# Optimization experiments

Hardware: AMD Instinct MI355X
Metric: run time of the kernel (lower is better)

Reference implementation:

```python
import jax, jax.numpy as jnp
import numpy as np
from functools import partial

N_NODES = 50000
N_EDGES = 1_600_000
T = 9
F_IN = 128
HID = 128
OUT = 1


def setup_inputs() -> dict:
    key = jax.random.key(0)
    ks = jax.random.split(key, 8)
    s = 0.05
    return {
        "x_seq": jax.random.normal(ks[0], (T, N_NODES, F_IN), dtype=jnp.float32),
        "edge_index": jax.random.randint(ks[1], (2, N_EDGES), 0, N_NODES, dtype=jnp.int64),
        "W_gcn": jax.random.normal(ks[2], (F_IN, HID), dtype=jnp.float32) * s,
        "b_gcn": jnp.zeros((HID,), dtype=jnp.float32),
        "W_ih": jax.random.normal(ks[3], (4 * HID, HID), dtype=jnp.float32) * s,
        "W_hh": jax.random.normal(ks[4], (4 * HID, HID), dtype=jnp.float32) * s,
        "b_ih": jnp.zeros((4 * HID,), dtype=jnp.float32),
        "b_hh": jnp.zeros((4 * HID,), dtype=jnp.float32),
        "W_fc": jax.random.normal(ks[5], (HID, OUT), dtype=jnp.float32) * s,
        "b_fc": jnp.zeros((OUT,), dtype=jnp.float32),
    }


def reference(x_seq, edge_index, W_gcn, b_gcn, W_ih, W_hh, b_ih, b_hh, W_fc, b_fc):
    T_, N, _ = x_seq.shape
    H = W_hh.shape[1]

    # --- GCNConv normalization (add self-loops, symmetric deg^-1/2) ---
    loops = jnp.arange(N, dtype=edge_index.dtype)
    src = jnp.concatenate([edge_index[0], loops])  # [E+N]
    dst = jnp.concatenate([edge_index[1], loops])  # [E+N]
    deg = jax.ops.segment_sum(jnp.ones_like(dst, dtype=x_seq.dtype), dst, num_segments=N)
    dinv = jnp.where(deg > 0, jax.lax.rsqrt(deg), 0.0)
    norm = dinv[src] * dinv[dst]  # [E+N]

    # Linear transform for all timesteps at once (dense GEMM)
    xw = jnp.einsum("tnf,fh->tnh", x_seq, W_gcn)  # [T, N, H]

    # Per-timestep gather -> scale -> scatter-add (scan to bound memory)
    def gcn_step(_, xw_t):
        msg = xw_t[src] * norm[:, None]                       # [E+N, H]
        agg = jax.ops.segment_sum(msg, dst, num_segments=N)   # [N, H]
        return None, jax.nn.relu(agg + b_gcn)                 # dropout: eval mode (identity)

    _, emb = jax.lax.scan(gcn_step, None, xw)  # [T, N, H]

    # --- single-layer LSTM over time, nodes as batch (PyTorch gate order i,f,g,o) ---
    def lstm_step(carry, x_t):
        h_prev, c_prev = carry
        gates = x_t @ W_ih.T + h_prev @ W_hh.T + (b_ih + b_hh)  # [N, 4H]
        i, f, g, o = jnp.split(gates, 4, axis=-1)
        i, f, o = jax.nn.sigmoid(i), jax.nn.sigmoid(f), jax.nn.sigmoid(o)
        g = jnp.tanh(g)
        c = f * c_prev + i * g
        h = o * jnp.tanh(c)
        return (h, c), h

    init = (jnp.zeros((N, H), x_seq.dtype), jnp.zeros((N, H), x_seq.dtype))
    _, hs = jax.lax.scan(lstm_step, init, emb)  # [T, N, H]

    lstm_out = jnp.transpose(hs, (1, 0, 2))  # [N, T, H] (batch_first)
    # final_dropout: eval mode (identity)
    return lstm_out @ W_fc + b_fc  # [N, T, OUT]
```

## Files before the change

### kernel.cpp

```cpp
#include <hip/hip_runtime.h>
#include <math.h>

#define NN 50000
#define TT 9
#define FD 128
#define HD 128

using short8 = __attribute__((ext_vector_type(8))) short;
using f32x4  = __attribute__((ext_vector_type(4))) float;
using half2v = __attribute__((ext_vector_type(2))) _Float16;
typedef unsigned short ushort_t;

__device__ inline unsigned short f2bf(float x) {
  unsigned int u = __float_as_uint(x);
  unsigned int r = (u + 0x7fffu + ((u >> 16) & 1u)) >> 16;
  return (unsigned short)r;
}
__device__ inline float bf2f(unsigned short h) {
  return __uint_as_float(((unsigned int)h) << 16);
}
__device__ inline void split2(float x, unsigned short& h, unsigned short& l) {
  h = f2bf(x);
  l = f2bf(x - bf2f(h));
}
__device__ inline float fast_sigmoid(float x) {
  x = fminf(fmaxf(x, -30.f), 30.f);
  return 1.f / (1.f + __expf(-x));
}
__device__ inline float fast_tanh(float x) {
  x = fminf(fmaxf(x, -15.f), 15.f);
  float e = __expf(2.f * x);
  return (e - 1.f) / (e + 1.f);
}

__global__ void k_detect(const unsigned int* __restrict__ e32, int nchk,
                         int* __restrict__ stride_out) {
  __shared__ unsigned int red[256];
  unsigned int acc = 0;
  for (int i = threadIdx.x; i < nchk; i += 256) acc |= e32[2 * i + 1];
  red[threadIdx.x] = acc;
  __syncthreads();
  for (int s = 128; s > 0; s >>= 1) {
    if ((int)threadIdx.x < s) red[threadIdx.x] |= red[threadIdx.x + s];
    __syncthreads();
  }
  if (threadIdx.x == 0) stride_out[0] = (red[0] == 0u) ? 2 : 1;
}

__global__ void k_count(const unsigned int* __restrict__ e32, int E,
                        const int* __restrict__ stridep, int* __restrict__ cnt) {
  int e = blockIdx.x * 256 + threadIdx.x;
  if (e >= E) return;
  int st = stridep[0];
  int d = (int)e32[(size_t)(E + e) * st];
  atomicAdd(&cnt[d], 1);
}

__global__ void k_dinv(const int* __restrict__ cnt, float* __restrict__ dinv, int N) {
  int n = blockIdx.x * 256 + threadIdx.x;
  if (n < N) dinv[n] = rsqrtf((float)(cnt[n] + 1));
}

__global__ void k_scan(const int* __restrict__ cnt, int* __restrict__ rowp, int N) {
  __shared__ int buf[1024];
  __shared__ int carry_s;
  if (threadIdx.x == 0) carry_s = 0;
  __syncthreads();
  for (int base = 0; base < N; base += 1024) {
    int i = base + threadIdx.x;
    int v = (i < N) ? cnt[i] : 0;
    buf[threadIdx.x] = v;
    __syncthreads();
    for (int off = 1; off < 1024; off <<= 1) {
      int t = ((int)threadIdx.x >= off) ? buf[threadIdx.x - off] : 0;
      __syncthreads();
      buf[threadIdx.x] += t;
      __syncthreads();
    }
    int incl = buf[threadIdx.x];
    int carry = carry_s;
    if (i < N) rowp[i] = carry + incl - v;
    __syncthreads();
    if (threadIdx.x == 1023) carry_s = carry + incl;
    __syncthreads();
  }
  if (threadIdx.x == 0) rowp[N] = carry_s;
}

__global__ void k_scatter(const unsigned int* __restrict__ e32, int E,
                          const int* __restrict__ stridep, const int* __restrict__ rowp,
                          int* __restrict__ fill, int* __restrict__ col) {
  int e = blockIdx.x * 256 + threadIdx.x;
  if (e >= E) return;
  int st = stridep[0];
  int s = (int)e32[(size_t)e * st];
  int d = (int)e32[(size_t)(E + e) * st];
  int pos = rowp[d] + atomicAdd(&fill[d], 1);
  col[pos] = s;
}

__global__ __launch_bounds__(256) void k_prep(const float* __restrict__ x,
                                              const float* __restrict__ dinv,
                                              _Float16* __restrict__ xs) {
  int lane = threadIdx.x & 63;
  int n = blockIdx.x * 4 + (threadIdx.x >> 6);
  int t = blockIdx.y;
  float dn = dinv[n];
  float2 v = *(const float2*)(x + ((size_t)t * NN + n) * 128 + lane * 2);
  half2v r;
  r.x = (_Float16)(v.x * dn);
  r.y = (_Float16)(v.y * dn);
  *(half2v*)(xs + ((size_t)t * NN + n) * 128 + lane * 2) = r;
}

__global__ void k_packw(const float* __restrict__ Wih, const float* __restrict__ Whh,
                        const float* __restrict__ bih, const float* __restrict__ bhh,
                        ushort_t* __restrict__ Wh_, ushort_t* __restrict__ Wl_,
                        float* __restrict__ bsum) {
  int r = blockIdx.x;
  int k = threadIdx.x;
  int ri = (r & 127) * 4 + (r >> 7);
  float v = (k < 128) ? Wih[(size_t)r * 128 + k] : Whh[(size_t)r * 128 + (k - 128)];
  unsigned short h, l;
  split2(v, h, l);
  size_t o = ((size_t)(k >> 3) * 512 + ri) * 8 + (k & 7);
  Wh_[o] = h;
  Wl_[o] = l;
  if (k == 0) bsum[ri] = bih[r] + bhh[r];
}

__global__ void k_packg(const float* __restrict__ Wg, ushort_t* __restrict__ Bh_,
                        ushort_t* __restrict__ Bl_) {
  int h = blockIdx.x, k = threadIdx.x;
  unsigned short hh, ll;
  split2(Wg[(size_t)k * 128 + h], hh, ll);
  size_t o = ((size_t)(k >> 3) * 128 + h) * 8 + (k & 7);
  Bh_[o] = hh;
  Bl_[o] = ll;
}

__global__ __launch_bounds__(256) void k_agg(const _Float16* __restrict__ xs,
                                             const float* __restrict__ dinv,
                                             const int* __restrict__ rowp,
                                             const int* __restrict__ col,
                                             ushort_t* __restrict__ agg_h,
                                             ushort_t* __restrict__ agg_l) {
  __shared__ unsigned int pk[4][128];
  int lane = threadIdx.x & 63;
  int wv = threadIdx.x >> 6;
  int n = blockIdx.x * 4 + wv;
  int t = blockIdx.y;
  const _Float16* xb = xs + (size_t)t * NN * 128;
  float dn = dinv[n];
  half2v sv = *(const half2v*)(xb + (size_t)n * 128 + lane * 2);
  float ax = (float)sv.x, ay = (float)sv.y;
  int beg = rowp[n], end = rowp[n + 1];
  for (int base = beg; base < end; base += 64) {
    int m = end - base;
    if (m > 64) m = 64;
    int sl = (lane < m) ? col[base + lane] : 0;
    int j = 0;
    for (; j + 8 <= m; j += 8) {
      int s[8];
#pragma unroll
      for (int u = 0; u < 8; ++u) s[u] = __shfl(sl, j + u);
      half2v g[8];
#pragma unroll
      for (int u = 0; u < 8; ++u)
        g[u] = *(const half2v*)(xb + (size_t)s[u] * 128 + lane * 2);
#pragma unroll
      for (int u = 0; u < 8; ++u) {
        ax += (float)g[u].x;
        ay += (float)g[u].y;
      }
    }
    for (; j < m; ++j) {
      int s = __shfl(sl, j);
      half2v g = *(const half2v*)(xb + (size_t)s * 128 + lane * 2);
      ax += (float)g.x;
      ay += (float)g.y;
    }
  }
  unsigned short hx, lx, hy, ly;
  split2(ax * dn, hx, lx);
  split2(ay * dn, hy, ly);
  pk[wv][lane * 2] = ((unsigned int)hx << 16) | lx;
  pk[wv][lane * 2 + 1] = ((unsigned int)hy << 16) | ly;
  __syncthreads();
  int tid = threadIdx.x;
  int chunk = tid >> 4, g = (tid >> 2) & 3, e2 = (tid & 3) * 2;
  unsigned int p0 = pk[g][chunk * 8 + e2];
  unsigned int p1 = pk[g][chunk * 8 + e2 + 1];
  int n2 = blockIdx.x * 4 + g;
  size_t ob = ((size_t)(chunk * 9 + t) * NN + n2) * 8 + e2;
  ushort2 vh, vl;
  vh.x = (unsigned short)(p0 >> 16);
  vh.y = (unsigned short)(p1 >> 16);
  vl.x = (unsigned short)(p0 & 0xffffu);
  vl.y = (unsigned short)(p1 & 0xffffu);
  *(ushort2*)(agg_h + ob) = vh;
  *(ushort2*)(agg_l + ob) = vl;
}

#define BN 48
__global__ __launch_bounds__(512, 4) void k_fused(
    const ushort_t* __restrict__ Ah_, const ushort_t* __restrict__ Al_,
    const ushort_t* __restrict__ Gh_, const ushort_t* __restrict__ Gl_,
    const float* __restrict__ bg, const ushort_t* __restrict__ Wh_,
    const ushort_t* __restrict__ Wl_, const float* __restrict__ bsum,
    const float* __restrict__ Wfc, const float* __restrict__ bfc,
    float* __restrict__ out) {
  __shared__ unsigned int ldsE[BN * 132];
  __shared__ unsigned int ldsH[BN * 132];
  __shared__ float obuf[8][BN];
  int tid = threadIdx.x;
  int w = tid >> 6, lane = tid & 63, q = lane >> 4, cl = lane & 15;
  int n0 = blockIdx.x * BN;
  const short8 zz = {0, 0, 0, 0, 0, 0, 0, 0};
  float cst[4][3] = {};
  float bfv = bfc[0];
#pragma unroll 1
  for (int t = 0; t < TT; ++t) {
    {
      f32x4 acce[3] = {};
#pragma unroll 1
      for (int ks = 0; ks < 4; ++ks) {
        int chunk = ks * 4 + q;
        size_t ao = ((size_t)chunk * 128 + w * 16 + cl) * 8;
        short8 gah = *(const short8*)(Gh_ + ao);
        short8 gal = *(const short8*)(Gl_ + ao);
#pragma unroll
        for (int ct = 0; ct < 3; ++ct) {
          int node = n0 + ct * 16 + cl;
          short8 bh = zz, bl = zz;
          if (node < NN) {
            size_t o = ((size_t)(chunk * 9 + t) * NN + node) * 8;
            bh = *(const short8*)(Ah_ + o);
            bl = *(const short8*)(Al_ + o);
          }
          acce[ct] = __builtin_amdgcn_mfma_f32_16x16x32_bf16(gah, bh, acce[ct], 0, 0, 0);
          acce[ct] = __builtin_amdgcn_mfma_f32_16x16x32_bf16(gah, bl, acce[ct], 0, 0, 0);
          acce[ct] = __builtin_amdgcn_mfma_f32_16x16x32_bf16(gal, bh, acce[ct], 0, 0, 0);
        }
      }
#pragma unroll
      for (int ct = 0; ct < 3; ++ct) {
#pragma unroll
        for (int j = 0; j < 4; ++j) {
          int hid = w * 16 + q * 4 + j;
          float v = acce[ct][j] + bg[hid];
          v = v > 0.f ? v : 0.f;
          unsigned short hh, hl;
          split2(v, hh, hl);
          ldsE[(ct * 16 + cl) * 132 + hid] = ((unsigned int)hh << 16) | hl;
        }
      }
    }
    __syncthreads();
    f32x4 acc[4][3] = {};
    int ksmax = (t == 0) ? 4 : 8;
#pragma unroll 1
    for (int ks = 0; ks < ksmax; ++ks) {
      int chunk = ks * 4 + q;
      const unsigned int* ldsB = (ks < 4) ? ldsE : ldsH;
      int kk = (ks & 3) * 32 + q * 8;
      short8 bh[3], bl[3];
#pragma unroll
      for (int ct = 0; ct < 3; ++ct) {
        const uint4* hp = (const uint4*)&ldsB[(ct * 16 + cl) * 132 + kk];
        uint4 ua = hp[0], ub = hp[1];
        union { unsigned int u[4]; short8 s; } rh, rl;
        rh.u[0] = __builtin_amdgcn_perm(ua.y, ua.x, 0x07060302u);
        rh.u[1] = __builtin_amdgcn_perm(ua.w, ua.z, 0x07060302u);
        rh.u[2] = __builtin_amdgcn_perm(ub.y, ub.x, 0x07060302u);
        rh.u[3] = __builtin_amdgcn_perm(ub.w, ub.z, 0x07060302u);
        rl.u[0] = __builtin_amdgcn_perm(ua.y, ua.x, 0x05040100u);
        rl.u[1] = __builtin_amdgcn_perm(ua.w, ua.z, 0x05040100u);
        rl.u[2] = __builtin_amdgcn_perm(ub.y, ub.x, 0x05040100u);
        rl.u[3] = __builtin_amdgcn_perm(ub.w, ub.z, 0x05040100u);
        bh[ct] = rh.s;
        bl[ct] = rl.s;
      }
#pragma unroll
      for (int rt = 0; rt < 4; ++rt) {
        size_t ao = ((size_t)chunk * 512 + w * 64 + rt * 16 + cl) * 8;
        short8 ah = *(const short8*)(Wh_ + ao);
        short8 al = *(const short8*)(Wl_ + ao);
#pragma unroll
        for (int ct = 0; ct < 3; ++ct) {
          acc[rt][ct] = __builtin_amdgcn_mfma_f32_16x16x32_bf16(ah, bh[ct], acc[rt][ct], 0, 0, 0);
          acc[rt][ct] = __builtin_amdgcn_mfma_f32_16x16x32_bf16(ah, bl[ct], acc[rt][ct], 0, 0, 0);
          acc[rt][ct] = __builtin_amdgcn_mfma_f32_16x16x32_bf16(al, bh[ct], acc[rt][ct], 0, 0, 0);
        }
      }
    }
    __syncthreads();
    float op[3] = {0.f, 0.f, 0.f};
#pragma unroll
    for (int rt = 0; rt < 4; ++rt) {
      int jl = w * 16 + rt * 4 + q;
      float4 bs = *(const float4*)(bsum + jl * 4);
      float wf = Wfc[jl];
#pragma unroll
      for (int ct = 0; ct < 3; ++ct) {
        float gi = acc[rt][ct][0] + bs.x;
        float gf = acc[rt][ct][1] + bs.y;
        float gg = acc[rt][ct][2] + bs.z;
        float go = acc[rt][ct][3] + bs.w;
        float ig = fast_sigmoid(gi), fg = fast_sigmoid(gf), og = fast_sigmoid(go);
        float gt = fast_tanh(gg);
        float cn = fg * cst[rt][ct] + ig * gt;
        cst[rt][ct] = cn;
        float hn = og * fast_tanh(cn);
        op[ct] += hn * wf;
        unsigned short hh, hl;
        split2(hn, hh, hl);
        ldsH[(ct * 16 + cl) * 132 + jl] = ((unsigned int)hh << 16) | hl;
      }
    }
#pragma unroll
    for (int ct = 0; ct < 3; ++ct) {
      op[ct] += __shfl_xor(op[ct], 16);
      op[ct] += __shfl_xor(op[ct], 32);
    }
    if (q == 0) {
#pragma unroll
      for (int ct = 0; ct < 3; ++ct) obuf[w][ct * 16 + cl] = op[ct];
    }
    __syncthreads();
    if (tid < BN) {
      int node = n0 + tid;
      if (node < NN) {
        float v = bfv;
#pragma unroll
        for (int ww = 0; ww < 8; ++ww) v += obuf[ww][tid];
        out[(size_t)node * TT + t] = v;
      }
    }
  }
}

static inline size_t alignup(size_t x) { return (x + 511) & ~(size_t)511; }

extern "C" void kernel_launch(void* const* d_in, const int* in_sizes, int n_in,
                              void* d_out, int out_size, void* d_ws, size_t ws_size,
                              hipStream_t stream) {
  const float* x_seq = (const float*)d_in[0];
  const unsigned int* e32 = (const unsigned int*)d_in[1];
  const float* W_gcn = (const float*)d_in[2];
  const float* b_gcn = (const float*)d_in[3];
  const float* W_ih = (const float*)d_in[4];
  const float* W_hh = (const float*)d_in[5];
  const float* b_ih = (const float*)d_in[6];
  const float* b_hh = (const float*)d_in[7];
  const float* W_fc = (const float*)d_in[8];
  const float* b_fc = (const float*)d_in[9];
  float* out = (float*)d_out;

  const int N = NN;
  const int E = in_sizes[1] / 2;

  char* p = (char*)d_ws;
  int* stridep = (int*)p;                    p += 512;
  int* cnt = (int*)p;                        p += alignup((size_t)N * 4);
  int* rowp = (int*)p;                       p += alignup((size_t)(N + 1) * 4);
  int* col = (int*)p;                        p += alignup((size_t)E * 4);
  float* dinv = (float*)p;                   p += alignup((size_t)N * 4);
  _Float16* xs16 = (_Float16*)p;             p += alignup((size_t)9 * N * 128 * 2);
  ushort_t* agg_h = (ushort_t*)p;            p += alignup((size_t)16 * 9 * N * 8 * 2);
  ushort_t* agg_l = (ushort_t*)p;            p += alignup((size_t)16 * 9 * N * 8 * 2);
  ushort_t* wpkh = (ushort_t*)p;             p += alignup((size_t)32 * 512 * 8 * 2);
  ushort_t* wpkl = (ushort_t*)p;             p += alignup((size_t)32 * 512 * 8 * 2);
  ushort_t* wgth = (ushort_t*)p;             p += alignup((size_t)16 * 128 * 8 * 2);
  ushort_t* wgtl = (ushort_t*)p;             p += alignup((size_t)16 * 128 * 8 * 2);
  float* bsum = (float*)p;                   p += alignup((size_t)512 * 4);

  hipMemsetAsync(cnt, 0, (size_t)N * 4, stream);

  int nchk = E < 8192 ? E : 8192;
  k_detect<<<1, 256, 0, stream>>>(e32, nchk, stridep);
  k_count<<<(E + 255) / 256, 256, 0, stream>>>(e32, E, stridep, cnt);
  k_dinv<<<(N + 255) / 256, 256, 0, stream>>>(cnt, dinv, N);
  k_scan<<<1, 1024, 0, stream>>>(cnt, rowp, N);
  hipMemsetAsync(cnt, 0, (size_t)N * 4, stream);
  k_scatter<<<(E + 255) / 256, 256, 0, stream>>>(e32, E, stridep, rowp, cnt, col);
  k_prep<<<dim3(N / 4, 9), 256, 0, stream>>>(x_seq, dinv, xs16);
  k_packw<<<512, 256, 0, stream>>>(W_ih, W_hh, b_ih, b_hh, wpkh, wpkl, bsum);
  k_packg<<<128, 128, 0, stream>>>(W_gcn, wgth, wgtl);

  k_agg<<<dim3(N / 4, 9), 256, 0, stream>>>(xs16, dinv, rowp, col, agg_h, agg_l);
  k_fused<<<(N + BN - 1) / BN, 512, 0, stream>>>(agg_h, agg_l, wgth, wgtl, b_gcn,
                                                 wpkh, wpkl, bsum, W_fc, b_fc, out);
}
```

Measured before the change: 1.442 ms.

## Aggregate all timesteps per node in one pass and split LDS hi/lo buffers

```diff
diff --git a/kernel.cpp b/kernel.cpp
--- a/kernel.cpp
+++ b/kernel.cpp
@@ -8,6 +8,7 @@
 
 using short8 = __attribute__((ext_vector_type(8))) short;
 using f32x4  = __attribute__((ext_vector_type(4))) float;
+using f32x2  = __attribute__((ext_vector_type(2))) float;
 using half2v = __attribute__((ext_vector_type(2))) _Float16;
 typedef unsigned short ushort_t;
 
@@ -106,7 +107,8 @@
   int n = blockIdx.x * 4 + (threadIdx.x >> 6);
   int t = blockIdx.y;
   float dn = dinv[n];
-  float2 v = *(const float2*)(x + ((size_t)t * NN + n) * 128 + lane * 2);
+  f32x2 v = __builtin_nontemporal_load(
+      (const f32x2*)(x + ((size_t)t * NN + n) * 128 + lane * 2));
   half2v r;
   r.x = (_Float16)(v.x * dn);
   r.y = (_Float16)(v.y * dn);
@@ -145,64 +147,85 @@
                                              const int* __restrict__ col,
                                              ushort_t* __restrict__ agg_h,
                                              ushort_t* __restrict__ agg_l) {
-  __shared__ unsigned int pk[4][128];
+  __shared__ unsigned int pk[4][9][130];
   int lane = threadIdx.x & 63;
   int wv = threadIdx.x >> 6;
   int n = blockIdx.x * 4 + wv;
-  int t = blockIdx.y;
-  const _Float16* xb = xs + (size_t)t * NN * 128;
   float dn = dinv[n];
-  half2v sv = *(const half2v*)(xb + (size_t)n * 128 + lane * 2);
-  float ax = (float)sv.x, ay = (float)sv.y;
+  float ax[9], ay[9];
+  {
+    const _Float16* xrow = xs + (size_t)n * 128 + lane * 2;
+#pragma unroll
+    for (int t = 0; t < 9; ++t) {
+      half2v sv = *(const half2v*)(xrow + (size_t)t * NN * 128);
+      ax[t] = (float)sv.x;
+      ay[t] = (float)sv.y;
+    }
+  }
   int beg = rowp[n], end = rowp[n + 1];
   for (int base = beg; base < end; base += 64) {
     int m = end - base;
     if (m > 64) m = 64;
     int sl = (lane < m) ? col[base + lane] : 0;
     int j = 0;
-    for (; j + 8 <= m; j += 8) {
-      int s[8];
-#pragma unroll
-      for (int u = 0; u < 8; ++u) s[u] = __shfl(sl, j + u);
-      half2v g[8];
-#pragma unroll
-      for (int u = 0; u < 8; ++u)
-        g[u] = *(const half2v*)(xb + (size_t)s[u] * 128 + lane * 2);
-#pragma unroll
-      for (int u = 0; u < 8; ++u) {
-        ax += (float)g[u].x;
-        ay += (float)g[u].y;
-      }
-    }
-    for (; j < m; ++j) {
-      int s = __shfl(sl, j);
-      half2v g = *(const half2v*)(xb + (size_t)s * 128 + lane * 2);
-      ax += (float)g.x;
-      ay += (float)g.y;
-    }
-  }
-  unsigned short hx, lx, hy, ly;
-  split2(ax * dn, hx, lx);
-  split2(ay * dn, hy, ly);
-  pk[wv][lane * 2] = ((unsigned int)hx << 16) | lx;
-  pk[wv][lane * 2 + 1] = ((unsigned int)hy << 16) | ly;
+    for (; j + 2 <= m; j += 2) {
+      int s0 = __shfl(sl, j), s1 = __shfl(sl, j + 1);
+      const _Float16* r0 = xs + (size_t)s0 * 128 + lane * 2;
+      const _Float16* r1 = xs + (size_t)s1 * 128 + lane * 2;
+      half2v g0[9], g1[9];
+#pragma unroll
+      for (int t = 0; t < 9; ++t) g0[t] = *(const half2v*)(r0 + (size_t)t * NN * 128);
+#pragma unroll
+      for (int t = 0; t < 9; ++t) g1[t] = *(const half2v*)(r1 + (size_t)t * NN * 128);
+#pragma unroll
+      for (int t = 0; t < 9; ++t) {
+        ax[t] += (float)g0[t].x + (float)g1[t].x;
+        ay[t] += (float)g0[t].y + (float)g1[t].y;
+      }
+    }
+    if (j < m) {
+      int s0 = __shfl(sl, j);
+      const _Float16* r0 = xs + (size_t)s0 * 128 + lane * 2;
+      half2v g0[9];
+#pragma unroll
+      for (int t = 0; t < 9; ++t) g0[t] = *(const half2v*)(r0 + (size_t)t * NN * 128);
+#pragma unroll
+      for (int t = 0; t < 9; ++t) {
+        ax[t] += (float)g0[t].x;
+        ay[t] += (float)g0[t].y;
+      }
+    }
+  }
+#pragma unroll
+  for (int t = 0; t < 9; ++t) {
+    unsigned short hx, lx, hy, ly;
+    split2(ax[t] * dn, hx, lx);
+    split2(ay[t] * dn, hy, ly);
+    pk[wv][t][lane * 2] = ((unsigned int)hx << 16) | lx;
+    pk[wv][t][lane * 2 + 1] = ((unsigned int)hy << 16) | ly;
+  }
   __syncthreads();
-  int tid = threadIdx.x;
-  int chunk = tid >> 4, g = (tid >> 2) & 3, e2 = (tid & 3) * 2;
-  unsigned int p0 = pk[g][chunk * 8 + e2];
-  unsigned int p1 = pk[g][chunk * 8 + e2 + 1];
-  int n2 = blockIdx.x * 4 + g;
-  size_t ob = ((size_t)(chunk * 9 + t) * NN + n2) * 8 + e2;
-  ushort2 vh, vl;
-  vh.x = (unsigned short)(p0 >> 16);
-  vh.y = (unsigned short)(p1 >> 16);
-  vl.x = (unsigned short)(p0 & 0xffffu);
-  vl.y = (unsigned short)(p1 & 0xffffu);
-  *(ushort2*)(agg_h + ob) = vh;
-  *(ushort2*)(agg_l + ob) = vl;
+  int n0 = blockIdx.x * 4;
+  for (int u = threadIdx.x; u < 576; u += 256) {
+    int g = u & 3, chunk = (u >> 2) & 15, t = u >> 6;
+    const unsigned int* src = &pk[g][t][chunk * 8];
+    unsigned int p[8];
+#pragma unroll
+    for (int e = 0; e < 8; ++e) p[e] = src[e];
+    union { unsigned int u4[4]; short8 s; } rh, rl;
+#pragma unroll
+    for (int k2 = 0; k2 < 4; ++k2) {
+      rh.u4[k2] = __builtin_amdgcn_perm(p[2 * k2 + 1], p[2 * k2], 0x07060302u);
+      rl.u4[k2] = __builtin_amdgcn_perm(p[2 * k2 + 1], p[2 * k2], 0x05040100u);
+    }
+    size_t o = ((size_t)(chunk * 9 + t) * NN + n0 + g) * 8;
+    __builtin_nontemporal_store(rh.s, (short8*)(agg_h + o));
+    __builtin_nontemporal_store(rl.s, (short8*)(agg_l + o));
+  }
 }
 
 #define BN 48
+#define LST 136
 __global__ __launch_bounds__(512, 4) void k_fused(
     const ushort_t* __restrict__ Ah_, const ushort_t* __restrict__ Al_,
     const ushort_t* __restrict__ Gh_, const ushort_t* __restrict__ Gl_,
@@ -210,8 +233,10 @@
     const ushort_t* __restrict__ Wl_, const float* __restrict__ bsum,
     const float* __restrict__ Wfc, const float* __restrict__ bfc,
     float* __restrict__ out) {
-  __shared__ unsigned int ldsE[BN * 132];
-  __shared__ unsigned int ldsH[BN * 132];
+  __shared__ ushort_t ldsEh[BN * LST];
+  __shared__ ushort_t ldsEl[BN * LST];
+  __shared__ ushort_t ldsHh[BN * LST];
+  __shared__ ushort_t ldsHl[BN * LST];
   __shared__ float obuf[8][BN];
   int tid = threadIdx.x;
   int w = tid >> 6, lane = tid & 63, q = lane >> 4, cl = lane & 15;
@@ -235,8 +260,8 @@
           short8 bh = zz, bl = zz;
           if (node < NN) {
             size_t o = ((size_t)(chunk * 9 + t) * NN + node) * 8;
-            bh = *(const short8*)(Ah_ + o);
-            bl = *(const short8*)(Al_ + o);
+            bh = __builtin_nontemporal_load((const short8*)(Ah_ + o));
+            bl = __builtin_nontemporal_load((const short8*)(Al_ + o));
           }
           acce[ct] = __builtin_amdgcn_mfma_f32_16x16x32_bf16(gah, bh, acce[ct], 0, 0, 0);
           acce[ct] = __builtin_amdgcn_mfma_f32_16x16x32_bf16(gah, bl, acce[ct], 0, 0, 0);
@@ -252,7 +277,9 @@
           v = v > 0.f ? v : 0.f;
           unsigned short hh, hl;
           split2(v, hh, hl);
-          ldsE[(ct * 16 + cl) * 132 + hid] = ((unsigned int)hh << 16) | hl;
+          int ro = (ct * 16 + cl) * LST + hid;
+          ldsEh[ro] = hh;
+          ldsEl[ro] = hl;
         }
       }
     }
@@ -262,24 +289,15 @@
 #pragma unroll 1
     for (int ks = 0; ks < ksmax; ++ks) {
       int chunk = ks * 4 + q;
-      const unsigned int* ldsB = (ks < 4) ? ldsE : ldsH;
+      const ushort_t* Bh = (ks < 4) ? ldsEh : ldsHh;
+      const ushort_t* Bl = (ks < 4) ? ldsEl : ldsHl;
       int kk = (ks & 3) * 32 + q * 8;
       short8 bh[3], bl[3];
 #pragma unroll
       for (int ct = 0; ct < 3; ++ct) {
-        const uint4* hp = (const uint4*)&ldsB[(ct * 16 + cl) * 132 + kk];
-        uint4 ua = hp[0], ub = hp[1];
-        union { unsigned int u[4]; short8 s; } rh, rl;
-        rh.u[0] = __builtin_amdgcn_perm(ua.y, ua.x, 0x07060302u);
-        rh.u[1] = __builtin_amdgcn_perm(ua.w, ua.z, 0x07060302u);
-        rh.u[2] = __builtin_amdgcn_perm(ub.y, ub.x, 0x07060302u);
-        rh.u[3] = __builtin_amdgcn_perm(ub.w, ub.z, 0x07060302u);
-        rl.u[0] = __builtin_amdgcn_perm(ua.y, ua.x, 0x05040100u);
-        rl.u[1] = __builtin_amdgcn_perm(ua.w, ua.z, 0x05040100u);
-        rl.u[2] = __builtin_amdgcn_perm(ub.y, ub.x, 0x05040100u);
-        rl.u[3] = __builtin_amdgcn_perm(ub.w, ub.z, 0x05040100u);
-        bh[ct] = rh.s;
-        bl[ct] = rl.s;
+        int ro = (ct * 16 + cl) * LST + kk;
+        bh[ct] = *(const short8*)(Bh + ro);
+        bl[ct] = *(const short8*)(Bl + ro);
       }
 #pragma unroll
       for (int rt = 0; rt < 4; ++rt) {
@@ -315,7 +333,9 @@
         op[ct] += hn * wf;
         unsigned short hh, hl;
         split2(hn, hh, hl);
-        ldsH[(ct * 16 + cl) * 132 + jl] = ((unsigned int)hh << 16) | hl;
+        int ro = (ct * 16 + cl) * LST + jl;
+        ldsHh[ro] = hh;
+        ldsHl[ro] = hl;
       }
     }
 #pragma unroll
@@ -388,7 +408,7 @@
   k_packw<<<512, 256, 0, stream>>>(W_ih, W_hh, b_ih, b_hh, wpkh, wpkl, bsum);
   k_packg<<<128, 128, 0, stream>>>(W_gcn, wgth, wgtl);
 
-  k_agg<<<dim3(N / 4, 9), 256, 0, stream>>>(xs16, dinv, rowp, col, agg_h, agg_l);
+  k_agg<<<N / 4, 256, 0, stream>>>(xs16, dinv, rowp, col, agg_h, agg_l);
   k_fused<<<(N + BN - 1) / BN, 512, 0, stream>>>(agg_h, agg_l, wgth, wgtl, b_gcn,
                                                  wpkh, wpkl, bsum, W_fc, b_fc, out);
 }
```

After: 1.619 ms. +12.2%, slower.

## Store aggregated features as single fp16 and widen fused LSTM tile to 96 nodes

Applied to the files above, without the earlier changes.

```diff
diff --git a/kernel.cpp b/kernel.cpp
--- a/kernel.cpp
+++ b/kernel.cpp
@@ -7,7 +7,9 @@
 #define HD 128
 
 using short8 = __attribute__((ext_vector_type(8))) short;
+using half8  = __attribute__((ext_vector_type(8))) _Float16;
 using f32x4  = __attribute__((ext_vector_type(4))) float;
+using f32x2  = __attribute__((ext_vector_type(2))) float;
 using half2v = __attribute__((ext_vector_type(2))) _Float16;
 typedef unsigned short ushort_t;
 
@@ -106,7 +108,8 @@
   int n = blockIdx.x * 4 + (threadIdx.x >> 6);
   int t = blockIdx.y;
   float dn = dinv[n];
-  float2 v = *(const float2*)(x + ((size_t)t * NN + n) * 128 + lane * 2);
+  f32x2 v = __builtin_nontemporal_load(
+      (const f32x2*)(x + ((size_t)t * NN + n) * 128 + lane * 2));
   half2v r;
   r.x = (_Float16)(v.x * dn);
   r.y = (_Float16)(v.y * dn);
@@ -129,23 +132,23 @@
   if (k == 0) bsum[ri] = bih[r] + bhh[r];
 }
 
-__global__ void k_packg(const float* __restrict__ Wg, ushort_t* __restrict__ Bh_,
-                        ushort_t* __restrict__ Bl_) {
+__global__ void k_packg(const float* __restrict__ Wg, _Float16* __restrict__ Gh_,
+                        _Float16* __restrict__ Gl_) {
   int h = blockIdx.x, k = threadIdx.x;
-  unsigned short hh, ll;
-  split2(Wg[(size_t)k * 128 + h], hh, ll);
+  float v = Wg[(size_t)k * 128 + h];
+  _Float16 hi = (_Float16)v;
+  _Float16 lo = (_Float16)(v - (float)hi);
   size_t o = ((size_t)(k >> 3) * 128 + h) * 8 + (k & 7);
-  Bh_[o] = hh;
-  Bl_[o] = ll;
+  Gh_[o] = hi;
+  Gl_[o] = lo;
 }
 
 __global__ __launch_bounds__(256) void k_agg(const _Float16* __restrict__ xs,
                                              const float* __restrict__ dinv,
                                              const int* __restrict__ rowp,
                                              const int* __restrict__ col,
-                                             ushort_t* __restrict__ agg_h,
-                                             ushort_t* __restrict__ agg_l) {
-  __shared__ unsigned int pk[4][128];
+                                             _Float16* __restrict__ agg16) {
+  __shared__ unsigned int pk[4][132];
   int lane = threadIdx.x & 63;
   int wv = threadIdx.x >> 6;
   int n = blockIdx.x * 4 + wv;
@@ -181,70 +184,66 @@
       ay += (float)g.y;
     }
   }
-  unsigned short hx, lx, hy, ly;
-  split2(ax * dn, hx, lx);
-  split2(ay * dn, hy, ly);
-  pk[wv][lane * 2] = ((unsigned int)hx << 16) | lx;
-  pk[wv][lane * 2 + 1] = ((unsigned int)hy << 16) | ly;
+  half2v r;
+  r.x = (_Float16)(ax * dn);
+  r.y = (_Float16)(ay * dn);
+  union { half2v h; unsigned int u; } cv;
+  cv.h = r;
+  pk[wv][lane] = cv.u;
   __syncthreads();
   int tid = threadIdx.x;
-  int chunk = tid >> 4, g = (tid >> 2) & 3, e2 = (tid & 3) * 2;
-  unsigned int p0 = pk[g][chunk * 8 + e2];
-  unsigned int p1 = pk[g][chunk * 8 + e2 + 1];
-  int n2 = blockIdx.x * 4 + g;
-  size_t ob = ((size_t)(chunk * 9 + t) * NN + n2) * 8 + e2;
-  ushort2 vh, vl;
-  vh.x = (unsigned short)(p0 >> 16);
-  vh.y = (unsigned short)(p1 >> 16);
-  vl.x = (unsigned short)(p0 & 0xffffu);
-  vl.y = (unsigned short)(p1 & 0xffffu);
-  *(ushort2*)(agg_h + ob) = vh;
-  *(ushort2*)(agg_l + ob) = vl;
-}
-
-#define BN 48
-__global__ __launch_bounds__(512, 4) void k_fused(
-    const ushort_t* __restrict__ Ah_, const ushort_t* __restrict__ Al_,
-    const ushort_t* __restrict__ Gh_, const ushort_t* __restrict__ Gl_,
-    const float* __restrict__ bg, const ushort_t* __restrict__ Wh_,
-    const ushort_t* __restrict__ Wl_, const float* __restrict__ bsum,
-    const float* __restrict__ Wfc, const float* __restrict__ bfc,
-    float* __restrict__ out) {
-  __shared__ unsigned int ldsE[BN * 132];
-  __shared__ unsigned int ldsH[BN * 132];
+  if (tid < 64) {
+    int g = tid & 3, c = tid >> 2;
+    uint4 u4;
+    u4.x = pk[g][c * 4 + 0];
+    u4.y = pk[g][c * 4 + 1];
+    u4.z = pk[g][c * 4 + 2];
+    u4.w = pk[g][c * 4 + 3];
+    int n2 = blockIdx.x * 4 + g;
+    *(uint4*)(agg16 + ((size_t)(c * 9 + t) * NN + n2) * 8) = u4;
+  }
+}
+
+#define BN 96
+#define LST 136
+__global__ __launch_bounds__(512, 2) void k_fused(
+    const _Float16* __restrict__ agg16, const _Float16* __restrict__ Gh_,
+    const _Float16* __restrict__ Gl_, const float* __restrict__ bg,
+    const ushort_t* __restrict__ Wh_, const ushort_t* __restrict__ Wl_,
+    const float* __restrict__ bsum, const float* __restrict__ Wfc,
+    const float* __restrict__ bfc, float* __restrict__ out) {
+  __shared__ ushort_t ldsEh[BN * LST];
+  __shared__ ushort_t ldsEl[BN * LST];
+  __shared__ ushort_t ldsHh[BN * LST];
+  __shared__ ushort_t ldsHl[BN * LST];
   __shared__ float obuf[8][BN];
   int tid = threadIdx.x;
   int w = tid >> 6, lane = tid & 63, q = lane >> 4, cl = lane & 15;
   int n0 = blockIdx.x * BN;
-  const short8 zz = {0, 0, 0, 0, 0, 0, 0, 0};
-  float cst[4][3] = {};
+  float cst[4][6] = {};
   float bfv = bfc[0];
 #pragma unroll 1
   for (int t = 0; t < TT; ++t) {
     {
-      f32x4 acce[3] = {};
-#pragma unroll 1
+      f32x4 acce[6] = {};
+#pragma unroll 2
       for (int ks = 0; ks < 4; ++ks) {
         int chunk = ks * 4 + q;
-        size_t ao = ((size_t)chunk * 128 + w * 16 + cl) * 8;
-        short8 gah = *(const short8*)(Gh_ + ao);
-        short8 gal = *(const short8*)(Gl_ + ao);
-#pragma unroll
-        for (int ct = 0; ct < 3; ++ct) {
+        size_t wo = ((size_t)chunk * 128 + w * 16 + cl) * 8;
+        half8 gah = *(const half8*)(Gh_ + wo);
+        half8 gal = *(const half8*)(Gl_ + wo);
+#pragma unroll
+        for (int ct = 0; ct < 6; ++ct) {
           int node = n0 + ct * 16 + cl;
-          short8 bh = zz, bl = zz;
-          if (node < NN) {
-            size_t o = ((size_t)(chunk * 9 + t) * NN + node) * 8;
-            bh = *(const short8*)(Ah_ + o);
-            bl = *(const short8*)(Al_ + o);
-          }
-          acce[ct] = __builtin_amdgcn_mfma_f32_16x16x32_bf16(gah, bh, acce[ct], 0, 0, 0);
-          acce[ct] = __builtin_amdgcn_mfma_f32_16x16x32_bf16(gah, bl, acce[ct], 0, 0, 0);
-          acce[ct] = __builtin_amdgcn_mfma_f32_16x16x32_bf16(gal, bh, acce[ct], 0, 0, 0);
+          half8 b = {0, 0, 0, 0, 0, 0, 0, 0};
+          if (node < NN)
+            b = *(const half8*)(agg16 + ((size_t)(chunk * 9 + t) * NN + node) * 8);
+          acce[ct] = __builtin_amdgcn_mfma_f32_16x16x32_f16(gah, b, acce[ct], 0, 0, 0);
+          acce[ct] = __builtin_amdgcn_mfma_f32_16x16x32_f16(gal, b, acce[ct], 0, 0, 0);
         }
       }
 #pragma unroll
-      for (int ct = 0; ct < 3; ++ct) {
+      for (int ct = 0; ct < 6; ++ct) {
 #pragma unroll
         for (int j = 0; j < 4; ++j) {
           int hid = w * 16 + q * 4 + j;
@@ -252,34 +251,27 @@
           v = v > 0.f ? v : 0.f;
           unsigned short hh, hl;
           split2(v, hh, hl);
-          ldsE[(ct * 16 + cl) * 132 + hid] = ((unsigned int)hh << 16) | hl;
+          int ro = (ct * 16 + cl) * LST + hid;
+          ldsEh[ro] = hh;
+          ldsEl[ro] = hl;
         }
       }
     }
     __syncthreads();
-    f32x4 acc[4][3] = {};
+    f32x4 acc[4][6] = {};
     int ksmax = (t == 0) ? 4 : 8;
-#pragma unroll 1
+#pragma unroll 2
     for (int ks = 0; ks < ksmax; ++ks) {
       int chunk = ks * 4 + q;
-      const unsigned int* ldsB = (ks < 4) ? ldsE : ldsH;
+      const ushort_t* Bh = (ks < 4) ? ldsEh : ldsHh;
+      const ushort_t* Bl = (ks < 4) ? ldsEl : ldsHl;
       int kk = (ks & 3) * 32 + q * 8;
-      short8 bh[3], bl[3];
-#pragma unroll
-      for (int ct = 0; ct < 3; ++ct) {
-        const uint4* hp = (const uint4*)&ldsB[(ct * 16 + cl) * 132 + kk];
-        uint4 ua = hp[0], ub = hp[1];
-        union { unsigned int u[4]; short8 s; } rh, rl;
-        rh.u[0] = __builtin_amdgcn_perm(ua.y, ua.x, 0x07060302u);
-        rh.u[1] = __builtin_amdgcn_perm(ua.w, ua.z, 0x07060302u);
-        rh.u[2] = __builtin_amdgcn_perm(ub.y, ub.x, 0x07060302u);
-        rh.u[3] = __builtin_amdgcn_perm(ub.w, ub.z, 0x07060302u);
-        rl.u[0] = __builtin_amdgcn_perm(ua.y, ua.x, 0x05040100u);
-        rl.u[1] = __builtin_amdgcn_perm(ua.w, ua.z, 0x05040100u);
-        rl.u[2] = __builtin_amdgcn_perm(ub.y, ub.x, 0x05040100u);
-        rl.u[3] = __builtin_amdgcn_perm(ub.w, ub.z, 0x05040100u);
-        bh[ct] = rh.s;
-        bl[ct] = rl.s;
+      short8 bh[6], bl[6];
+#pragma unroll
+      for (int ct = 0; ct < 6; ++ct) {
+        int ro = (ct * 16 + cl) * LST + kk;
+        bh[ct] = *(const short8*)(Bh + ro);
+        bl[ct] = *(const short8*)(Bl + ro);
       }
 #pragma unroll
       for (int rt = 0; rt < 4; ++rt) {
@@ -287,7 +279,7 @@
         short8 ah = *(const short8*)(Wh_ + ao);
         short8 al = *(const short8*)(Wl_ + ao);
 #pragma unroll
-        for (int ct = 0; ct < 3; ++ct) {
+        for (int ct = 0; ct < 6; ++ct) {
           acc[rt][ct] = __builtin_amdgcn_mfma_f32_16x16x32_bf16(ah, bh[ct], acc[rt][ct], 0, 0, 0);
           acc[rt][ct] = __builtin_amdgcn_mfma_f32_16x16x32_bf16(ah, bl[ct], acc[rt][ct], 0, 0, 0);
           acc[rt][ct] = __builtin_amdgcn_mfma_f32_16x16x32_bf16(al, bh[ct], acc[rt][ct], 0, 0, 0);
@@ -295,14 +287,14 @@
       }
     }
     __syncthreads();
-    float op[3] = {0.f, 0.f, 0.f};
+    float op[6] = {0.f, 0.f, 0.f, 0.f, 0.f, 0.f};
 #pragma unroll
     for (int rt = 0; rt < 4; ++rt) {
       int jl = w * 16 + rt * 4 + q;
       float4 bs = *(const float4*)(bsum + jl * 4);
       float wf = Wfc[jl];
 #pragma unroll
-      for (int ct = 0; ct < 3; ++ct) {
+      for (int ct = 0; ct < 6; ++ct) {
         float gi = acc[rt][ct][0] + bs.x;
         float gf = acc[rt][ct][1] + bs.y;
         float gg = acc[rt][ct][2] + bs.z;
@@ -315,17 +307,19 @@
         op[ct] += hn * wf;
         unsigned short hh, hl;
         split2(hn, hh, hl);
-        ldsH[(ct * 16 + cl) * 132 + jl] = ((unsigned int)hh << 16) | hl;
-      }
-    }
-#pragma unroll
-    for (int ct = 0; ct < 3; ++ct) {
+        int ro = (ct * 16 + cl) * LST + jl;
+        ldsHh[ro] = hh;
+        ldsHl[ro] = hl;
+      }
+    }
+#pragma unroll
+    for (int ct = 0; ct < 6; ++ct) {
       op[ct] += __shfl_xor(op[ct], 16);
       op[ct] += __shfl_xor(op[ct], 32);
     }
     if (q == 0) {
 #pragma unroll
-      for (int ct = 0; ct < 3; ++ct) obuf[w][ct * 16 + cl] = op[ct];
+      for (int ct = 0; ct < 6; ++ct) obuf[w][ct * 16 + cl] = op[ct];
     }
     __syncthreads();
     if (tid < BN) {
@@ -367,12 +361,11 @@
   int* col = (int*)p;                        p += alignup((size_t)E * 4);
   float* dinv = (float*)p;                   p += alignup((size_t)N * 4);
   _Float16* xs16 = (_Float16*)p;             p += alignup((size_t)9 * N * 128 * 2);
-  ushort_t* agg_h = (ushort_t*)p;            p += alignup((size_t)16 * 9 * N * 8 * 2);
-  ushort_t* agg_l = (ushort_t*)p;            p += alignup((size_t)16 * 9 * N * 8 * 2);
+  _Float16* agg16 = (_Float16*)p;            p += alignup((size_t)16 * 9 * N * 8 * 2);
   ushort_t* wpkh = (ushort_t*)p;             p += alignup((size_t)32 * 512 * 8 * 2);
   ushort_t* wpkl = (ushort_t*)p;             p += alignup((size_t)32 * 512 * 8 * 2);
-  ushort_t* wgth = (ushort_t*)p;             p += alignup((size_t)16 * 128 * 8 * 2);
-  ushort_t* wgtl = (ushort_t*)p;             p += alignup((size_t)16 * 128 * 8 * 2);
+  _Float16* wgth = (_Float16*)p;             p += alignup((size_t)16 * 128 * 8 * 2);
+  _Float16* wgtl = (_Float16*)p;             p += alignup((size_t)16 * 128 * 8 * 2);
   float* bsum = (float*)p;                   p += alignup((size_t)512 * 4);
 
   hipMemsetAsync(cnt, 0, (size_t)N * 4, stream);
@@ -388,7 +381,7 @@
   k_packw<<<512, 256, 0, stream>>>(W_ih, W_hh, b_ih, b_hh, wpkh, wpkl, bsum);
   k_packg<<<128, 128, 0, stream>>>(W_gcn, wgth, wgtl);
 
-  k_agg<<<dim3(N / 4, 9), 256, 0, stream>>>(xs16, dinv, rowp, col, agg_h, agg_l);
-  k_fused<<<(N + BN - 1) / BN, 512, 0, stream>>>(agg_h, agg_l, wgth, wgtl, b_gcn,
+  k_agg<<<dim3(N / 4, 9), 256, 0, stream>>>(xs16, dinv, rowp, col, agg16);
+  k_fused<<<(N + BN - 1) / BN, 512, 0, stream>>>(agg16, wgth, wgtl, b_gcn,
                                                  wpkh, wpkl, bsum, W_fc, b_fc, out);
 }
```

New measurement: 1.704 ms. 18.1% more time.
